# Optimization experiments

Measured on AMD Instinct MI355X. Metric: run time of the kernel, lower is better.

Reference implementation:

```python
import jax, jax.numpy as jnp
import numpy as np

B, T, D = 4, 2048, 2048
H = 16
KD = D // 2          # key_dim = expand_k * d_model
VD = D               # value_dim = expand_v * d_model
DK = KD // H         # head_k_dim = 64
DV = VD // H         # head_v_dim = 128
LR = 16              # gate_low_rank_dim
EPS = 1e-5
GATE_LOGIT_NORMALIZER = 16.0


def setup_inputs() -> dict:
    key = jax.random.key(0)
    ks = jax.random.split(key, 9)
    def w(k, shape):
        fan_in = shape[0]
        return (jax.random.normal(k, shape, jnp.float32) * (fan_in ** -0.5)).astype(jnp.float32)
    return {
        "x":      jax.random.normal(ks[0], (B, T, D), jnp.float32),
        "Wq":     w(ks[1], (D, KD)),
        "Wk":     w(ks[2], (D, KD)),
        "Wv":     w(ks[3], (D, VD)),
        "Wg":     w(ks[4], (D, VD)),      # output gate projection
        "Wgk1":   w(ks[5], (D, LR)),      # gk low-rank down-proj (no bias)
        "Wgk2":   w(ks[6], (LR, KD)),     # gk up-proj
        "bgk2":   jnp.zeros((KD,), jnp.float32),
        "norm_w": jnp.ones((DV,), jnp.float32),  # per-head RMSNorm weight
        "Wo":     w(ks[7], (VD, D)),
    }


def reference(x, Wq, Wk, Wv, Wg, Wgk1, Wgk2, bgk2, norm_w, Wo):
    b, t, _ = x.shape
    dv = norm_w.shape[0]
    vd = Wv.shape[1]
    h = vd // dv
    dk = Wq.shape[1] // h
    scale = dk ** -0.5

    q = (x @ Wq).reshape(b, t, h, dk) * scale
    k = (x @ Wk).reshape(b, t, h, dk)
    v = (x @ Wv).reshape(b, t, h, dv)
    # forget gate: logsigmoid(low_rank_proj(x)) / gate_logit_normalizer
    gk = jax.nn.log_sigmoid((x @ Wgk1) @ Wgk2 + bgk2) / GATE_LOGIT_NORMALIZER
    gk = gk.reshape(b, t, h, dk)

    # time-major for scan: [T, B, H, d]
    qT = jnp.moveaxis(q, 1, 0)
    kT = jnp.moveaxis(k, 1, 0)
    vT = jnp.moveaxis(v, 1, 0)
    gT = jnp.moveaxis(gk, 1, 0)

    def step(S, inp):
        qt, kt, vt, gt = inp
        # S_t = diag(exp(gk_t)) S_{t-1} + k_t^T v_t ; shape [B,H,DK,DV]
        S = S * jnp.exp(gt)[..., None] + kt[..., None] * vt[..., None, :]
        ot = jnp.einsum('bhk,bhkv->bhv', qt, S)
        return S, ot

    S0 = jnp.zeros((b, h, dk, dv), x.dtype)
    _, o = jax.lax.scan(step, S0, (qT, kT, vT, gT))
    o = jnp.moveaxis(o, 0, 1)  # [B, T, H, DV]

    # FusedRMSNormSwishGate: rmsnorm(o) * weight * swish(g), per head dim
    g = (x @ Wg).reshape(b, t, h, dv)
    o = o * jax.lax.rsqrt(jnp.mean(o * o, axis=-1, keepdims=True) + EPS) * norm_w
    o = o * (g * jax.nn.sigmoid(g))
    return o.reshape(b, t, vd) @ Wo
```

## Files before the change

### kernel.cpp

```cpp
#include <hip/hip_runtime.h>
#include <hip/hip_bf16.h>
#include <type_traits>


using bf16x8 = __attribute__((ext_vector_type(8))) short;
using f32x4  = __attribute__((ext_vector_type(4))) float;
using f32x16 = __attribute__((ext_vector_type(16))) float;

static __device__ __forceinline__ float bf2f(ushort u) {
  union { unsigned int i; float f; } v;
  v.i = ((unsigned int)u) << 16;
  return v.f;
}
static __device__ __forceinline__ ushort f2bf(float f) {
  __hip_bfloat16 h = __float2bfloat16(f);
  return *reinterpret_cast<ushort*>(&h);
}
static __device__ __forceinline__ unsigned int pack2(float lo, float hi) {
  return (unsigned int)f2bf(lo) | ((unsigned int)f2bf(hi) << 16);
}
static __device__ __forceinline__ void unpack8(uint4 v, float* f) {
  f[0] = bf2f((ushort)(v.x & 0xffff)); f[1] = bf2f((ushort)(v.x >> 16));
  f[2] = bf2f((ushort)(v.y & 0xffff)); f[3] = bf2f((ushort)(v.y >> 16));
  f[4] = bf2f((ushort)(v.z & 0xffff)); f[5] = bf2f((ushort)(v.z >> 16));
  f[6] = bf2f((ushort)(v.w & 0xffff)); f[7] = bf2f((ushort)(v.w >> 16));
}

#define GLDS16(g, l) __builtin_amdgcn_global_load_lds( \
    (const __attribute__((address_space(1))) unsigned int*)(g), \
    (__attribute__((address_space(3))) unsigned int*)(l), 16, 0, 0)

#define SWZ3(row) ((((row) & 1) << 2) | (((row) >> 1) & 3))

#define GC_CUMSUM(gc, th)                                              \
  {                                                                    \
    const int k_ = (th) & 63, seg_ = (th) >> 6;                        \
    float s_ = 0.f;                                                    \
    _Pragma("unroll")                                                  \
    for (int i_ = 0; i_ < 16; ++i_) {                                  \
      s_ += gc[seg_ * 16 + i_][k_];                                    \
      gc[seg_ * 16 + i_][k_] = s_;                                     \
    }                                                                  \
    __syncthreads();                                                   \
    float t0_ = gc[15][k_], t1_ = gc[31][k_], t2_ = gc[47][k_];        \
    __syncthreads();                                                   \
    float off_ = (seg_ > 0 ? t0_ : 0.f) + (seg_ > 1 ? t1_ : 0.f) +     \
                 (seg_ > 2 ? t2_ : 0.f);                               \
    if (seg_) {                                                        \
      _Pragma("unroll")                                                \
      for (int i_ = 0; i_ < 16; ++i_) gc[seg_ * 16 + i_][k_] += off_;  \
    }                                                                  \
    __syncthreads();                                                   \
  }

__global__ __launch_bounds__(256) void f32_to_bf16(
    const float* __restrict__ in, ushort* __restrict__ out, long n) {
  long i = ((long)blockIdx.x * 256 + threadIdx.x) * 8;
  if (i >= n) return;
  float4 a = *(const float4*)(in + i);
  float4 b = *(const float4*)(in + i + 4);
  uint4 o;
  o.x = pack2(a.x, a.y); o.y = pack2(a.z, a.w);
  o.z = pack2(b.x, b.y); o.w = pack2(b.z, b.w);
  *(uint4*)(out + i) = o;
}

__global__ __launch_bounds__(256) void transpose_f32_bf16(
    const float* __restrict__ in, ushort* __restrict__ out, int R, int C) {
  __shared__ float tile[64][65];
  const int t = threadIdx.x;
  const int tc = blockIdx.x * 64;
  const int tr = blockIdx.y * 64;
  const int lr = t >> 2;
  const int lc = (t & 3) * 16;
  const float* ip = in + (long)(tr + lr) * C + tc + lc;
#pragma unroll
  for (int j = 0; j < 4; ++j)
    *(float4*)(&tile[lr][lc + j * 4]) = *(const float4*)(ip + j * 4);
  __syncthreads();
  const int c = t >> 2;
  const int r0 = (t & 3) * 16;
  ushort tmp[16];
#pragma unroll
  for (int j = 0; j < 16; ++j) tmp[j] = f2bf(tile[r0 + j][c]);
  ushort* op = out + (long)(tc + c) * R + tr + r0;
  *(uint4*)(op)     = *(uint4*)(tmp);
  *(uint4*)(op + 8) = *(uint4*)(tmp + 8);
}

template <typename OT>
__global__ __launch_bounds__(512, 2) void gemm_bt8(
    const ushort* __restrict__ A, const ushort* __restrict__ BT,
    OT* __restrict__ C, int M, int N, int K) {
  __shared__ ushort sA[2 * 16384];
  __shared__ ushort sB[2 * 16384];
  const int t = threadIdx.x;
  const int nbx = N >> 8;
  const int cpx = gridDim.x >> 3;
  const int wg = ((int)blockIdx.x & 7) * cpx + ((int)blockIdx.x >> 3);
  const int brow = (wg / nbx) * 256;
  const int bcol = (wg % nbx) * 256;

  const int w = t >> 6, l = t & 63;
  const int wm = w >> 2, wn = w & 3;
  const int l31 = l & 31, l5 = l >> 5;
  const int NT = K >> 6;

  const int srow = t >> 3;
  const int cswz = ((t & 7) ^ SWZ3(srow)) * 8;
  const ushort* Abase = A + (size_t)(brow + srow) * K + cswz;
  const ushort* Bbase = BT + (size_t)(bcol + srow) * K + cswz;
  const int t8 = t * 8;

  auto stageA = [&](int bb, int hh, int jt) {
    const ushort* s = Abase + (size_t)(hh * 128) * K + jt * 64;
    ushort* d = sA + bb * 16384 + hh * 8192 + t8;
    GLDS16(s, d);
    GLDS16(s + (size_t)64 * K, d + 4096);
  };
  auto stageB = [&](int bb, int hh, int jt) {
    const ushort* s = Bbase + (size_t)(hh * 128) * K + jt * 64;
    ushort* d = sB + bb * 16384 + hh * 8192 + t8;
    GLDS16(s, d);
    GLDS16(s + (size_t)64 * K, d + 4096);
  };

  const int swz = SWZ3(l31 & 7);
  const int aRow = (wm * 32 + l31) * 64;
  const int bRow = (wn * 32 + l31) * 64;
#define KSL(ks) ((((ks) * 2 + l5) ^ swz) * 8)

  f32x16 acc[4][2];
#pragma unroll
  for (int m = 0; m < 4; ++m)
#pragma unroll
    for (int n = 0; n < 2; ++n)
#pragma unroll
      for (int r = 0; r < 16; ++r) acc[m][n][r] = 0.f;

  stageA(0, 0, 0); stageB(0, 0, 0); stageB(0, 1, 0); stageA(0, 1, 0);
  asm volatile("s_waitcnt vmcnt(4)" ::: "memory");
  stageA(1, 0, 1); stageB(1, 0, 1); stageB(1, 1, 1);
  asm volatile("s_waitcnt vmcnt(6)" ::: "memory");
  __builtin_amdgcn_s_barrier();

  for (int kt = 0; kt < NT; ++kt) {
    const int bb = kt & 1;
    const int aOff = bb * 16384, bOff = bb * 16384;
    bf16x8 aF[2][4], bF[2][4];

#pragma unroll
    for (int mf = 0; mf < 2; ++mf)
#pragma unroll
      for (int ks = 0; ks < 4; ++ks)
        aF[mf][ks] = *(const bf16x8*)(sA + aOff + mf * 4096 + aRow + KSL(ks));
#pragma unroll
    for (int ks = 0; ks < 4; ++ks)
      bF[0][ks] = *(const bf16x8*)(sB + bOff + bRow + KSL(ks));
    if (kt + 1 < NT) stageA(bb ^ 1, 1, kt + 1);
    __builtin_amdgcn_s_barrier();
    __builtin_amdgcn_s_setprio(1);
#pragma unroll
    for (int mf = 0; mf < 2; ++mf)
#pragma unroll
      for (int ks = 0; ks < 4; ++ks)
        acc[mf][0] = __builtin_amdgcn_mfma_f32_32x32x16_bf16(aF[mf][ks], bF[0][ks], acc[mf][0], 0, 0, 0);
    __builtin_amdgcn_s_setprio(0);
    __builtin_amdgcn_s_barrier();

#pragma unroll
    for (int ks = 0; ks < 4; ++ks)
      bF[1][ks] = *(const bf16x8*)(sB + bOff + 8192 + bRow + KSL(ks));
    if (kt + 2 < NT) stageA(bb, 0, kt + 2);
    __builtin_amdgcn_s_barrier();
    __builtin_amdgcn_s_setprio(1);
#pragma unroll
    for (int mf = 0; mf < 2; ++mf)
#pragma unroll
      for (int ks = 0; ks < 4; ++ks)
        acc[mf][1] = __builtin_amdgcn_mfma_f32_32x32x16_bf16(aF[mf][ks], bF[1][ks], acc[mf][1], 0, 0, 0);
    __builtin_amdgcn_s_setprio(0);
    __builtin_amdgcn_s_barrier();

#pragma unroll
    for (int mf = 0; mf < 2; ++mf)
#pragma unroll
      for (int ks = 0; ks < 4; ++ks)
        aF[mf][ks] = *(const bf16x8*)(sA + aOff + 8192 + mf * 4096 + aRow + KSL(ks));
    if (kt + 2 < NT) stageB(bb, 0, kt + 2);
    __builtin_amdgcn_s_barrier();
    __builtin_amdgcn_s_setprio(1);
#pragma unroll
    for (int mf = 0; mf < 2; ++mf)
#pragma unroll
      for (int ks = 0; ks < 4; ++ks)
        acc[2 + mf][0] = __builtin_amdgcn_mfma_f32_32x32x16_bf16(aF[mf][ks], bF[0][ks], acc[2 + mf][0], 0, 0, 0);
    __builtin_amdgcn_s_setprio(0);
    __builtin_amdgcn_s_barrier();

    if (kt + 2 < NT) stageB(bb, 1, kt + 2);
    __builtin_amdgcn_s_barrier();
    __builtin_amdgcn_s_setprio(1);
#pragma unroll
    for (int mf = 0; mf < 2; ++mf)
#pragma unroll
      for (int ks = 0; ks < 4; ++ks)
        acc[2 + mf][1] = __builtin_amdgcn_mfma_f32_32x32x16_bf16(aF[mf][ks], bF[1][ks], acc[2 + mf][1], 0, 0, 0);
    __builtin_amdgcn_s_setprio(0);
    if (kt < NT - 2)       asm volatile("s_waitcnt vmcnt(6)" ::: "memory");
    else if (kt == NT - 2) asm volatile("s_waitcnt vmcnt(0)" ::: "memory");
    __builtin_amdgcn_s_barrier();
  }
#undef KSL

#pragma unroll
  for (int mf = 0; mf < 4; ++mf)
#pragma unroll
    for (int nf = 0; nf < 2; ++nf) {
      long col = bcol + nf * 128 + wn * 32 + l31;
      long rbase = brow + mf * 64 + wm * 32 + 4 * l5;
#pragma unroll
      for (int r = 0; r < 16; ++r) {
        long row = rbase + (r & 3) + 8 * (r >> 2);
        if constexpr (std::is_same_v<OT, ushort>) C[row * N + col] = f2bf(acc[mf][nf][r]);
        else                                      C[row * N + col] = acc[mf][nf][r];
      }
    }
}

__global__ __launch_bounds__(256) void gate_kernel(
    const ushort* __restrict__ xb, const float* __restrict__ Wgk1,
    const float* __restrict__ Wgk2, const float* __restrict__ bgk2,
    ushort* __restrict__ gbuf) {
  const long m0 = (long)blockIdx.x * 8;
  const int t = threadIdx.x;
  __shared__ float sx[8][2048];
  __shared__ float red[16][8][16];
  __shared__ float z1[8][16];
#pragma unroll
  for (int u = 0; u < 8; ++u) {
    int idx = (u * 256 + t) * 8;
    int r = idx >> 11, cc = idx & 2047;
    uint4 v = *(const uint4*)(xb + (m0 + r) * 2048 + cc);
    float f[8];
    unpack8(v, f);
    *(float4*)(&sx[r][cc])     = (float4){f[0], f[1], f[2], f[3]};
    *(float4*)(&sx[r][cc + 4]) = (float4){f[4], f[5], f[6], f[7]};
  }
  __syncthreads();
  const int j = t & 15, dg = t >> 4;
  float a8[8] = {0.f, 0.f, 0.f, 0.f, 0.f, 0.f, 0.f, 0.f};
  const float* wp = Wgk1 + (dg * 128) * 16 + j;
  for (int dc = 0; dc < 128; dc += 4) {
    float w0 = wp[(dc + 0) * 16], w1 = wp[(dc + 1) * 16];
    float w2 = wp[(dc + 2) * 16], w3 = wp[(dc + 3) * 16];
    const int dd = dg * 128 + dc;
#pragma unroll
    for (int r = 0; r < 8; ++r) {
      float4 xv = *(const float4*)(&sx[r][dd]);
      a8[r] += xv.x * w0 + xv.y * w1 + xv.z * w2 + xv.w * w3;
    }
  }
#pragma unroll
  for (int r = 0; r < 8; ++r) red[dg][r][j] = a8[r];
  __syncthreads();
  if (t < 128) {
    int r = t >> 4, jj = t & 15;
    float s = 0.f;
#pragma unroll
    for (int g = 0; g < 16; ++g) s += red[g][r][jj];
    z1[r][jj] = s;
  }
  __syncthreads();
#pragma unroll
  for (int q = 0; q < 4; ++q) {
    int n = q * 256 + t;
    float w2v[16];
#pragma unroll
    for (int l2 = 0; l2 < 16; ++l2) w2v[l2] = Wgk2[l2 * 1024 + n];
    float bb = bgk2[n];
#pragma unroll
    for (int r = 0; r < 8; ++r) {
      float a = bb;
#pragma unroll
      for (int l2 = 0; l2 < 16; ++l2) a += z1[r][l2] * w2v[l2];
      float ls = fminf(a, 0.f) - log1pf(__expf(-fabsf(a)));
      gbuf[(m0 + r) * 1024 + n] = f2bf(ls * 0.0625f);
    }
  }
}

__global__ __launch_bounds__(256) void chunk_contrib_kernel(
    const ushort* __restrict__ qkvg, const ushort* __restrict__ gbuf,
    ushort* __restrict__ STbuf, float* __restrict__ EGtot) {
  const int blk = blockIdx.x;
  const int bh = blk >> 5, c = blk & 31;
  const int b = bh >> 4, h = bh & 15;
  const long row0 = (long)b * 2048 + c * 64;
  const int th = threadIdx.x;

  __shared__ float  gc[64][65];
  __shared__ ushort khT[64][72];
  __shared__ ushort vT[128][72];

  {
    const int t = th >> 2;
    const int k0 = (th & 3) * 16;
    const ushort* gp = gbuf + (row0 + t) * 1024 + h * 64 + k0;
    uint4 a = *(const uint4*)gp;
    uint4 b4 = *(const uint4*)(gp + 8);
    float f[8];
    unpack8(a, f);
#pragma unroll
    for (int j = 0; j < 8; ++j) gc[t][k0 + j] = f[j];
    unpack8(b4, f);
#pragma unroll
    for (int j = 0; j < 8; ++j) gc[t][k0 + 8 + j] = f[j];
  }
  __syncthreads();
  GC_CUMSUM(gc, th)
  if (th < 64) EGtot[(long)blk * 64 + th] = __expf(gc[63][th]);

  {
    const int s = th & 63, kq = th >> 6;
    const ushort* kp = qkvg + (row0 + s) * 6144 + 1024 + h * 64 + kq * 16;
    uint4 a = *(const uint4*)kp;
    uint4 b4 = *(const uint4*)(kp + 8);
    float f[16];
    unpack8(a, f); unpack8(b4, f + 8);
#pragma unroll
    for (int j = 0; j < 16; ++j) {
      int k = kq * 16 + j;
      khT[k][s] = f2bf(f[j] * __expf(gc[63][k] - gc[s][k]));
    }
    const ushort* vp = qkvg + (row0 + s) * 6144 + 2048 + h * 128 + kq * 32;
#pragma unroll
    for (int u = 0; u < 4; ++u) {
      uint4 vv = *(const uint4*)(vp + u * 8);
      const ushort* pv = (const ushort*)&vv;
#pragma unroll
      for (int j = 0; j < 8; ++j) vT[kq * 32 + u * 8 + j][s] = pv[j];
    }
  }
  __syncthreads();

  const int w = th >> 6, l = th & 63;
  const int lr = l & 15, kq8 = (l >> 4) * 8;
  f32x4 acc[4][2];
#pragma unroll
  for (int m = 0; m < 4; ++m)
#pragma unroll
    for (int n = 0; n < 2; ++n) acc[m][n] = (f32x4){0.f, 0.f, 0.f, 0.f};
#pragma unroll
  for (int ks = 0; ks < 64; ks += 32) {
#pragma unroll
    for (int m = 0; m < 4; ++m) {
      bf16x8 af = *(const bf16x8*)(&khT[m * 16 + lr][ks + kq8]);
#pragma unroll
      for (int n = 0; n < 2; ++n) {
        bf16x8 bv = *(const bf16x8*)(&vT[w * 32 + n * 16 + lr][ks + kq8]);
        acc[m][n] = __builtin_amdgcn_mfma_f32_16x16x32_bf16(af, bv, acc[m][n], 0, 0, 0);
      }
    }
  }
  ushort* Cc = STbuf + (long)blk * 8192;
  const int rq = (l >> 4) * 4;
#pragma unroll
  for (int m = 0; m < 4; ++m)
#pragma unroll
    for (int n = 0; n < 2; ++n) {
      int dv = w * 32 + n * 16 + lr;
      ushort tmp[4];
#pragma unroll
      for (int r = 0; r < 4; ++r) tmp[r] = f2bf(acc[m][n][r]);
      *(uint2*)(Cc + dv * 64 + m * 16 + rq) = *(uint2*)tmp;
    }
}

__global__ __launch_bounds__(256) void chunk_scan_kernel(
    ushort* __restrict__ STbuf, const float* __restrict__ EGtot) {
  const int blk = blockIdx.x;
  const int bh = blk >> 2, qd = blk & 3;
  const int th = threadIdx.x;
  const int dv = qd * 32 + (th >> 3);
  const int k0 = (th & 7) * 8;
  ushort* base = STbuf + (long)bh * 32 * 8192 + dv * 64 + k0;
  const float* eg = EGtot + (long)bh * 32 * 64 + k0;
  float S[8];
#pragma unroll
  for (int i = 0; i < 8; ++i) S[i] = 0.f;
  uint4 cv = *(const uint4*)base;
  float4 e0 = *(const float4*)(eg);
  float4 e1 = *(const float4*)(eg + 4);
  for (int c = 0; c < 32; ++c) {
    ushort* cur = base;
    base += 8192; eg += 64;
    uint4 nv = cv; float4 n0 = e0, n1 = e1;
    if (c < 31) {
      nv = *(const uint4*)base;
      n0 = *(const float4*)(eg);
      n1 = *(const float4*)(eg + 4);
    }
    float cf[8];
    unpack8(cv, cf);
    float ee[8] = {e0.x, e0.y, e0.z, e0.w, e1.x, e1.y, e1.z, e1.w};
    ushort so[8];
#pragma unroll
    for (int i = 0; i < 8; ++i) {
      so[i] = f2bf(S[i]);
      S[i] = S[i] * ee[i] + cf[i];
    }
    *(uint4*)cur = *(uint4*)so;
    cv = nv; e0 = n0; e1 = n1;
  }
}

__global__ __launch_bounds__(256) void chunk_output_kernel(
    const ushort* __restrict__ qkvg, const ushort* __restrict__ gbuf,
    const ushort* __restrict__ STbuf, const float* __restrict__ norm_w,
    ushort* __restrict__ oo) {
  const int blk = blockIdx.x;
  const int bh = blk >> 5, c = blk & 31;
  const int b = bh >> 4, h = bh & 15;
  const long row0 = (long)b * 2048 + c * 64;
  const int th = threadIdx.x;

  __shared__ __align__(16) char pool[71936];
  float  (*gc)[65]  = (float(*)[65])(pool);
  ushort (*qg)[72]  = (ushort(*)[72])(pool + 16640);
  ushort (*kg)[72]  = (ushort(*)[72])(pool + 25856);
  ushort (*vT)[72]  = (ushort(*)[72])(pool + 35072);
  ushort (*STs)[72] = (ushort(*)[72])(pool + 53504);
  ushort (*P)[72]   = (ushort(*)[72])(pool);

  {
    const int t = th >> 2;
    const int k0 = (th & 3) * 16;
    const ushort* gp = gbuf + (row0 + t) * 1024 + h * 64 + k0;
    uint4 a = *(const uint4*)gp;
    uint4 b4 = *(const uint4*)(gp + 8);
    float f[8];
    unpack8(a, f);
#pragma unroll
    for (int j = 0; j < 8; ++j) gc[t][k0 + j] = f[j];
    unpack8(b4, f);
#pragma unroll
    for (int j = 0; j < 8; ++j) gc[t][k0 + 8 + j] = f[j];

    const ushort* qp = qkvg + (row0 + t) * 6144 + h * 64 + k0;
    *(uint4*)(&qg[t][k0])     = *(const uint4*)qp;
    *(uint4*)(&qg[t][k0 + 8]) = *(const uint4*)(qp + 8);
    const ushort* kp = qp + 1024;
    *(uint4*)(&kg[t][k0])     = *(const uint4*)kp;
    *(uint4*)(&kg[t][k0 + 8]) = *(const uint4*)(kp + 8);
  }
  {
    const int s = th & 63, kq = th >> 6;
    const ushort* vp = qkvg + (row0 + s) * 6144 + 2048 + h * 128 + kq * 32;
#pragma unroll
    for (int u = 0; u < 4; ++u) {
      uint4 vv = *(const uint4*)(vp + u * 8);
      const ushort* pv = (const ushort*)&vv;
#pragma unroll
      for (int j = 0; j < 8; ++j) vT[kq * 32 + u * 8 + j][s] = pv[j];
    }
  }
  {
    const int row = th >> 1;
    const int col0 = (th & 1) * 32;
    const ushort* sp = STbuf + (long)blk * 8192 + row * 64 + col0;
#pragma unroll
    for (int u = 0; u < 4; ++u)
      *(uint4*)(&STs[row][col0 + u * 8]) = *(const uint4*)(sp + u * 8);
  }
  __syncthreads();
  GC_CUMSUM(gc, th)
  {
    const int t = th & 63, kb = (th >> 6) * 16;
#pragma unroll
    for (int u = 0; u < 2; ++u) {
      uint4 qv = *(const uint4*)(&qg[t][kb + u * 8]);
      uint4 kv = *(const uint4*)(&kg[t][kb + u * 8]);
      float qf[8], kf[8];
      unpack8(qv, qf); unpack8(kv, kf);
      ushort qo[8], ko[8];
#pragma unroll
      for (int j = 0; j < 8; ++j) {
        float g = gc[t][kb + u * 8 + j];
        qo[j] = f2bf(qf[j] * __expf(g) * 0.125f);
        ko[j] = f2bf(kf[j] * __expf(-g));
      }
      *(uint4*)(&qg[t][kb + u * 8]) = *(uint4*)qo;
      *(uint4*)(&kg[t][kb + u * 8]) = *(uint4*)ko;
    }
  }
  __syncthreads();

  const int w = th >> 6, l = th & 63;
  const int lr = l & 15, kq8 = (l >> 4) * 8;
  const int rq = (l >> 4) * 4;

  f32x4 acc1[4];
#pragma unroll
  for (int n = 0; n < 4; ++n) acc1[n] = (f32x4){0.f, 0.f, 0.f, 0.f};
#pragma unroll
  for (int kk = 0; kk < 64; kk += 32) {
    bf16x8 af = *(const bf16x8*)(&qg[w * 16 + lr][kk + kq8]);
#pragma unroll
    for (int n = 0; n < 4; ++n) {
      bf16x8 bv = *(const bf16x8*)(&kg[n * 16 + lr][kk + kq8]);
      acc1[n] = __builtin_amdgcn_mfma_f32_16x16x32_bf16(af, bv, acc1[n], 0, 0, 0);
    }
  }
#pragma unroll
  for (int n = 0; n < 4; ++n) {
    int s = n * 16 + lr;
#pragma unroll
    for (int r = 0; r < 4; ++r) {
      int t = w * 16 + rq + r;
      P[t][s] = f2bf(s <= t ? acc1[n][r] : 0.f);
    }
  }
  __syncthreads();

  f32x4 acc2[8];
#pragma unroll
  for (int n = 0; n < 8; ++n) acc2[n] = (f32x4){0.f, 0.f, 0.f, 0.f};
#pragma unroll
  for (int ks = 0; ks < 64; ks += 32) {
    bf16x8 af = *(const bf16x8*)(&P[w * 16 + lr][ks + kq8]);
#pragma unroll
    for (int n = 0; n < 8; ++n) {
      bf16x8 bv = *(const bf16x8*)(&vT[n * 16 + lr][ks + kq8]);
      acc2[n] = __builtin_amdgcn_mfma_f32_16x16x32_bf16(af, bv, acc2[n], 0, 0, 0);
    }
  }
#pragma unroll
  for (int kk = 0; kk < 64; kk += 32) {
    bf16x8 af = *(const bf16x8*)(&qg[w * 16 + lr][kk + kq8]);
#pragma unroll
    for (int n = 0; n < 8; ++n) {
      bf16x8 bv = *(const bf16x8*)(&STs[n * 16 + lr][kk + kq8]);
      acc2[n] = __builtin_amdgcn_mfma_f32_16x16x32_bf16(af, bv, acc2[n], 0, 0, 0);
    }
  }

  float gv[8][4];
#pragma unroll
  for (int n = 0; n < 8; ++n) {
    int dv = n * 16 + lr;
#pragma unroll
    for (int r = 0; r < 4; ++r)
      gv[n][r] = bf2f(qkvg[(row0 + w * 16 + rq + r) * 6144 + 4096 + h * 128 + dv]);
  }

  float sumsq[4] = {0.f, 0.f, 0.f, 0.f};
#pragma unroll
  for (int n = 0; n < 8; ++n)
#pragma unroll
    for (int r = 0; r < 4; ++r) sumsq[r] += acc2[n][r] * acc2[n][r];
#pragma unroll
  for (int d = 1; d < 16; d <<= 1)
#pragma unroll
    for (int r = 0; r < 4; ++r) sumsq[r] += __shfl_xor(sumsq[r], d);
  float inv[4];
#pragma unroll
  for (int r = 0; r < 4; ++r) inv[r] = rsqrtf(sumsq[r] * (1.f / 128.f) + 1e-5f);

#pragma unroll
  for (int n = 0; n < 8; ++n) {
    int dv = n * 16 + lr;
    float nw = norm_w[dv];
#pragma unroll
    for (int r = 0; r < 4; ++r) {
      float g = gv[n][r];
      float sw = g / (1.f + __expf(-g));
      oo[(row0 + w * 16 + rq + r) * 2048 + h * 128 + dv] =
          f2bf(acc2[n][r] * inv[r] * nw * sw);
    }
  }
}

extern "C" void kernel_launch(void* const* d_in, const int* in_sizes, int n_in,
                              void* d_out, int out_size, void* d_ws, size_t ws_size,
                              hipStream_t stream) {
  const float* x      = (const float*)d_in[0];
  const float* Wq     = (const float*)d_in[1];
  const float* Wk     = (const float*)d_in[2];
  const float* Wv     = (const float*)d_in[3];
  const float* Wg     = (const float*)d_in[4];
  const float* Wgk1   = (const float*)d_in[5];
  const float* Wgk2   = (const float*)d_in[6];
  const float* bgk2   = (const float*)d_in[7];
  const float* norm_w = (const float*)d_in[8];
  const float* Wo     = (const float*)d_in[9];
  float* out = (float*)d_out;

  char* ws = (char*)d_ws;
  ushort* WT    = (ushort*)(ws);
  ushort* WoT   = (ushort*)(ws + 25165824);
  ushort* qkvg  = (ushort*)(ws + 33554432);
  ushort* gbuf  = (ushort*)(ws + 134217728);
  ushort* STbuf = (ushort*)(ws + 150994944);
  ushort* xb    = (ushort*)(ws + 150994944);
  float*  EGtot = (float*)(ws + 184549376);
  ushort* oo    = (ushort*)(ws + 185073664);

  dim3 blk(256);
  f32_to_bf16<<<dim3(8192), blk, 0, stream>>>(x, xb, (long)8192 * 2048);
  transpose_f32_bf16<<<dim3(16, 32), blk, 0, stream>>>(Wq, WT, 2048, 1024);
  transpose_f32_bf16<<<dim3(16, 32), blk, 0, stream>>>(Wk, WT + (size_t)1024 * 2048, 2048, 1024);
  transpose_f32_bf16<<<dim3(32, 32), blk, 0, stream>>>(Wv, WT + (size_t)2048 * 2048, 2048, 2048);
  transpose_f32_bf16<<<dim3(32, 32), blk, 0, stream>>>(Wg, WT + (size_t)4096 * 2048, 2048, 2048);
  transpose_f32_bf16<<<dim3(32, 32), blk, 0, stream>>>(Wo, WoT, 2048, 2048);

  gemm_bt8<ushort><<<dim3(768), dim3(512), 0, stream>>>(xb, WT, qkvg, 8192, 6144, 2048);
  gate_kernel<<<dim3(1024), blk, 0, stream>>>(xb, Wgk1, Wgk2, bgk2, gbuf);

  chunk_contrib_kernel<<<dim3(2048), blk, 0, stream>>>(qkvg, gbuf, STbuf, EGtot);
  chunk_scan_kernel<<<dim3(256), blk, 0, stream>>>(STbuf, EGtot);
  chunk_output_kernel<<<dim3(2048), blk, 0, stream>>>(qkvg, gbuf, STbuf, norm_w, oo);

  gemm_bt8<float><<<dim3(256), dim3(512), 0, stream>>>(oo, WoT, out, 8192, 2048, 2048);
}
```

Measured before the change: 464.7 us.

## Fuse x bf16 conversion into gate kernel, merge weight transposes, tighten GEMM waits

The gate kernel now reads fp32 x directly and writes the bf16 copy of x while computing the low-rank gate, which removes the separate conversion pass and the re-read of the bf16 x. The four Wq/Wk/Wv/Wg transposes are merged into one launch to cut launch overhead and tail effects. In the GEMM main loop, explicit lgkmcnt waits and sched_barriers are added around the barriers to control where LDS reads are waited on and to stop the compiler moving code across them. This could serialize LDS latency differently and change MFMA overlap.

```diff
diff --git a/kernel.cpp b/kernel.cpp
--- a/kernel.cpp
+++ b/kernel.cpp
@@ -53,16 +53,34 @@
     __syncthreads();                                                   \
   }
 
-__global__ __launch_bounds__(256) void f32_to_bf16(
-    const float* __restrict__ in, ushort* __restrict__ out, long n) {
-  long i = ((long)blockIdx.x * 256 + threadIdx.x) * 8;
-  if (i >= n) return;
-  float4 a = *(const float4*)(in + i);
-  float4 b = *(const float4*)(in + i + 4);
-  uint4 o;
-  o.x = pack2(a.x, a.y); o.y = pack2(a.z, a.w);
-  o.z = pack2(b.x, b.y); o.w = pack2(b.z, b.w);
-  *(uint4*)(out + i) = o;
+__global__ __launch_bounds__(256) void transpose_w4(
+    const float* __restrict__ Wq, const float* __restrict__ Wk,
+    const float* __restrict__ Wv, const float* __restrict__ Wg,
+    ushort* __restrict__ WT) {
+  const int bx = blockIdx.x;
+  const float* src; int srcC, colbase, outrow0;
+  if (bx < 16)      { src = Wq; srcC = 1024; colbase = bx * 64;        outrow0 = 0; }
+  else if (bx < 32) { src = Wk; srcC = 1024; colbase = (bx - 16) * 64; outrow0 = 1024; }
+  else if (bx < 64) { src = Wv; srcC = 2048; colbase = (bx - 32) * 64; outrow0 = 2048; }
+  else              { src = Wg; srcC = 2048; colbase = (bx - 64) * 64; outrow0 = 4096; }
+  __shared__ float tile[64][65];
+  const int t = threadIdx.x;
+  const int tr = blockIdx.y * 64;
+  const int lr = t >> 2;
+  const int lc = (t & 3) * 16;
+  const float* ip = src + (long)(tr + lr) * srcC + colbase + lc;
+#pragma unroll
+  for (int j = 0; j < 4; ++j)
+    *(float4*)(&tile[lr][lc + j * 4]) = *(const float4*)(ip + j * 4);
+  __syncthreads();
+  const int c = t >> 2;
+  const int r0 = (t & 3) * 16;
+  ushort tmp[16];
+#pragma unroll
+  for (int j = 0; j < 16; ++j) tmp[j] = f2bf(tile[r0 + j][c]);
+  ushort* op = WT + (long)(outrow0 + colbase + c) * 2048 + tr + r0;
+  *(uint4*)(op)     = *(uint4*)(tmp);
+  *(uint4*)(op + 8) = *(uint4*)(tmp + 8);
 }
 
 __global__ __launch_bounds__(256) void transpose_f32_bf16(
@@ -158,7 +176,10 @@
     for (int ks = 0; ks < 4; ++ks)
       bF[0][ks] = *(const bf16x8*)(sB + bOff + bRow + KSL(ks));
     if (kt + 1 < NT) stageA(bb ^ 1, 1, kt + 1);
-    __builtin_amdgcn_s_barrier();
+    asm volatile("s_waitcnt lgkmcnt(8)" ::: "memory");
+    __builtin_amdgcn_s_barrier();
+    asm volatile("s_waitcnt lgkmcnt(0)" ::: "memory");
+    __builtin_amdgcn_sched_barrier(0);
     __builtin_amdgcn_s_setprio(1);
 #pragma unroll
     for (int mf = 0; mf < 2; ++mf)
@@ -173,6 +194,8 @@
       bF[1][ks] = *(const bf16x8*)(sB + bOff + 8192 + bRow + KSL(ks));
     if (kt + 2 < NT) stageA(bb, 0, kt + 2);
     __builtin_amdgcn_s_barrier();
+    asm volatile("s_waitcnt lgkmcnt(0)" ::: "memory");
+    __builtin_amdgcn_sched_barrier(0);
     __builtin_amdgcn_s_setprio(1);
 #pragma unroll
     for (int mf = 0; mf < 2; ++mf)
@@ -189,6 +212,8 @@
         aF[mf][ks] = *(const bf16x8*)(sA + aOff + 8192 + mf * 4096 + aRow + KSL(ks));
     if (kt + 2 < NT) stageB(bb, 0, kt + 2);
     __builtin_amdgcn_s_barrier();
+    asm volatile("s_waitcnt lgkmcnt(0)" ::: "memory");
+    __builtin_amdgcn_sched_barrier(0);
     __builtin_amdgcn_s_setprio(1);
 #pragma unroll
     for (int mf = 0; mf < 2; ++mf)
@@ -200,6 +225,7 @@
 
     if (kt + 2 < NT) stageB(bb, 1, kt + 2);
     __builtin_amdgcn_s_barrier();
+    __builtin_amdgcn_sched_barrier(0);
     __builtin_amdgcn_s_setprio(1);
 #pragma unroll
     for (int mf = 0; mf < 2; ++mf)
@@ -229,9 +255,9 @@
 }
 
 __global__ __launch_bounds__(256) void gate_kernel(
-    const ushort* __restrict__ xb, const float* __restrict__ Wgk1,
+    const float* __restrict__ x, const float* __restrict__ Wgk1,
     const float* __restrict__ Wgk2, const float* __restrict__ bgk2,
-    ushort* __restrict__ gbuf) {
+    ushort* __restrict__ xb, ushort* __restrict__ gbuf) {
   const long m0 = (long)blockIdx.x * 8;
   const int t = threadIdx.x;
   __shared__ float sx[8][2048];
@@ -241,11 +267,15 @@
   for (int u = 0; u < 8; ++u) {
     int idx = (u * 256 + t) * 8;
     int r = idx >> 11, cc = idx & 2047;
-    uint4 v = *(const uint4*)(xb + (m0 + r) * 2048 + cc);
-    float f[8];
-    unpack8(v, f);
-    *(float4*)(&sx[r][cc])     = (float4){f[0], f[1], f[2], f[3]};
-    *(float4*)(&sx[r][cc + 4]) = (float4){f[4], f[5], f[6], f[7]};
+    const float* xp = x + (m0 + r) * 2048 + cc;
+    float4 a = *(const float4*)xp;
+    float4 b = *(const float4*)(xp + 4);
+    *(float4*)(&sx[r][cc])     = a;
+    *(float4*)(&sx[r][cc + 4]) = b;
+    uint4 o;
+    o.x = pack2(a.x, a.y); o.y = pack2(a.z, a.w);
+    o.z = pack2(b.x, b.y); o.w = pack2(b.z, b.w);
+    *(uint4*)(xb + (m0 + r) * 2048 + cc) = o;
   }
   __syncthreads();
   const int j = t & 15, dg = t >> 4;
@@ -607,15 +637,11 @@
   ushort* oo    = (ushort*)(ws + 185073664);
 
   dim3 blk(256);
-  f32_to_bf16<<<dim3(8192), blk, 0, stream>>>(x, xb, (long)8192 * 2048);
-  transpose_f32_bf16<<<dim3(16, 32), blk, 0, stream>>>(Wq, WT, 2048, 1024);
-  transpose_f32_bf16<<<dim3(16, 32), blk, 0, stream>>>(Wk, WT + (size_t)1024 * 2048, 2048, 1024);
-  transpose_f32_bf16<<<dim3(32, 32), blk, 0, stream>>>(Wv, WT + (size_t)2048 * 2048, 2048, 2048);
-  transpose_f32_bf16<<<dim3(32, 32), blk, 0, stream>>>(Wg, WT + (size_t)4096 * 2048, 2048, 2048);
+  gate_kernel<<<dim3(1024), blk, 0, stream>>>(x, Wgk1, Wgk2, bgk2, xb, gbuf);
+  transpose_w4<<<dim3(96, 32), blk, 0, stream>>>(Wq, Wk, Wv, Wg, WT);
   transpose_f32_bf16<<<dim3(32, 32), blk, 0, stream>>>(Wo, WoT, 2048, 2048);
 
   gemm_bt8<ushort><<<dim3(768), dim3(512), 0, stream>>>(xb, WT, qkvg, 8192, 6144, 2048);
-  gate_kernel<<<dim3(1024), blk, 0, stream>>>(xb, Wgk1, Wgk2, bgk2, gbuf);
 
   chunk_contrib_kernel<<<dim3(2048), blk, 0, stream>>>(qkvg, gbuf, STbuf, EGtot);
   chunk_scan_kernel<<<dim3(256), blk, 0, stream>>>(STbuf, EGtot);
```

New measurement: 456.0 us. About the same (-1.9%).
